# Kernel tuning notes

Measured on AMD Instinct MI355X. Metric: run time of the kernel, lower is better.

Reference implementation:

```python
import jax, jax.numpy as jnp
import numpy as np

PE_SIZE = 16

def sinusoidal_pe(d, t):
    # standard transformer sinusoidal positional encoding [t, d]
    pos = jnp.arange(t, dtype=jnp.float32)[:, None]
    div = jnp.exp(jnp.arange(0, d, 2, dtype=jnp.float32) * (-jnp.log(10000.0) / d))
    pe = jnp.zeros((t, d), dtype=jnp.float32)
    pe = pe.at[:, 0::2].set(jnp.sin(pos * div))
    pe = pe.at[:, 1::2].set(jnp.cos(pos * div))
    return pe

def setup_inputs() -> dict:
    key = jax.random.key(0)
    ks = jax.random.split(key, 12)
    B, T, N, F = 2, 256, 128, 16
    E, D, H = 1024, 128, 288
    inp = {
        'spikes': jax.random.normal(ks[0], (B, T, N, F), dtype=jnp.float32),
        'W_emb': jax.random.normal(ks[1], (F, D), dtype=jnp.float32) * (1.0 / np.sqrt(F)),
        'b_emb': jnp.zeros((D,), dtype=jnp.float32),
        'Ws1': jax.random.normal(ks[2], (D, D), dtype=jnp.float32) * (1.0 / np.sqrt(D)),
        'bs1': jnp.zeros((D,), dtype=jnp.float32),
        'Ws2': jax.random.normal(ks[3], (D, D), dtype=jnp.float32) * (1.0 / np.sqrt(D)),
        'bs2': jnp.zeros((D,), dtype=jnp.float32),
        'Wr1': jax.random.normal(ks[4], (D, D), dtype=jnp.float32) * (1.0 / np.sqrt(D)),
        'br1': jnp.zeros((D,), dtype=jnp.float32),
        'Wr2': jax.random.normal(ks[5], (D, D), dtype=jnp.float32) * (1.0 / np.sqrt(D)),
        'br2': jnp.zeros((D,), dtype=jnp.float32),
        'Wc1': jax.random.normal(ks[6], (H, H), dtype=jnp.float32) * (1.0 / np.sqrt(H)),
        'bc1': jnp.zeros((H,), dtype=jnp.float32),
        'Wc2': jax.random.normal(ks[7], (H, 5), dtype=jnp.float32) * (1.0 / np.sqrt(H)),
        'bc2': jnp.zeros((5,), dtype=jnp.float32),
        'send_edges': jax.random.randint(ks[8], (E,), 0, N, dtype=jnp.int64 if jax.config.read('jax_enable_x64') else jnp.int32),
        'recv_edges': jax.random.randint(ks[9], (E,), 0, N, dtype=jnp.int64 if jax.config.read('jax_enable_x64') else jnp.int32),
    }
    return inp

def reference(spikes, W_emb, b_emb, Ws1, bs1, Ws2, bs2, Wr1, br1, Wr2, br2,
              Wc1, bc1, Wc2, bc2, send_edges, recv_edges):
    b, t = spikes.shape[0], spikes.shape[1]
    # embedder: Linear feat->emb (shared for send/recv inputs)
    emb = spikes @ W_emb + b_emb                       # [b,t,N,D]
    # send/recv MLPs: ReLU after every Linear (2 layers)
    send = jax.nn.relu(jax.nn.relu(emb @ Ws1 + bs1) @ Ws2 + bs2)  # [b,t,N,D]
    recv = jax.nn.relu(jax.nn.relu(emb @ Wr1 + br1) @ Wr2 + br2)  # [b,t,N,D]
    # edge gather along node dim
    send_e = send[:, :, send_edges]                    # [b,t,E,D]
    recv_e = recv[:, :, recv_edges]                    # [b,t,E,D]
    # positional encoding, broadcast over batch and edges
    pe = sinusoidal_pe(PE_SIZE, t)                     # [t,PE]
    pe_b = jnp.broadcast_to(pe[None, :, None, :], (b, t, send_e.shape[2], PE_SIZE))
    send_cat = jnp.concatenate([send_e, pe_b], axis=-1)
    recv_cat = jnp.concatenate([recv_e, pe_b], axis=-1)
    # temporal offset pairing: sender at t+1, receiver at t
    full_emb = jnp.concatenate([send_cat[:, 1:], recv_cat[:, :-1]], axis=-1)  # [b,t-1,E,288]
    # combine MLP: Linear+ReLU, Linear (final bias zero-init, no activation)
    out = jax.nn.relu(full_emb @ Wc1 + bc1) @ Wc2 + bc2   # [b,t-1,E,5]
    return out
```

## Files before the change

kernel.cpp:

```cpp
#include <hip/hip_runtime.h>
#include <hip/hip_bf16.h>
#include <hip/hip_fp16.h>
#include <cstdint>
#include <cstddef>

typedef __attribute__((ext_vector_type(8))) short bf16x8;
typedef __attribute__((ext_vector_type(8))) _Float16 f16x8;
typedef __attribute__((ext_vector_type(4))) float f32x4;
typedef __attribute__((ext_vector_type(4))) unsigned u32x4;

__device__ inline unsigned short f2bf(float f) {
    __hip_bfloat16 h = __float2bfloat16(f);
    return __builtin_bit_cast(unsigned short, h);
}
__device__ inline unsigned short f2h(float f) {
    _Float16 h = (_Float16)f;
    return __builtin_bit_cast(unsigned short, h);
}
__device__ inline unsigned cvtpkrtz(float lo, float hi) {
    unsigned pk;
    asm("v_cvt_pkrtz_f16_f32 %0, %1, %2" : "=v"(pk) : "v"(lo), "v"(hi));
    return pk;
}

__global__ void prep_kernel(
    const float* __restrict__ W_emb, const float* __restrict__ b_emb,
    const float* __restrict__ Ws1, const float* __restrict__ bs1,
    const float* __restrict__ Wr1, const float* __restrict__ br1,
    const float* __restrict__ Ws2, const float* __restrict__ bs2,
    const float* __restrict__ Wr2, const float* __restrict__ br2,
    const float* __restrict__ Wc1, const float* __restrict__ bc1,
    const float* __restrict__ Wc2,
    float* __restrict__ P, float* __restrict__ bias1, float* __restrict__ bias2,
    unsigned short* __restrict__ wg1f, unsigned short* __restrict__ wg2f,
    unsigned short* __restrict__ wg3fT, unsigned short* __restrict__ wc2f)
{
    const int tid = threadIdx.x;

    if (blockIdx.x < 287) {
        __shared__ float sv[3][16], cv[3][16];
        const int base = blockIdx.x * 256;
        const int t0 = base / 288;
        if (tid < 48) {
            const int dt = tid >> 4, i = tid & 15;
            const int ii = i >> 1;
            const float div = expf(-1.1512925464970229f * (float)ii);
            const float ang = (float)(t0 + dt) * div;
            sv[dt][i] = sinf(ang);
            cv[dt][i] = cosf(ang);
        }
        __syncthreads();
        const int id = base + tid;
        if (id < 73440) {
            const int t = id / 288, ho = id % 288;
            const int dt = t - t0;
            float acc = bc1[ho];
#pragma unroll
            for (int i = 0; i < 8; i++) {
                acc += sv[dt + 1][2 * i] * Wc1[(size_t)(128 + 2 * i) * 288 + ho];
                acc += cv[dt + 1][2 * i] * Wc1[(size_t)(129 + 2 * i) * 288 + ho];
                acc += sv[dt][2 * i]     * Wc1[(size_t)(272 + 2 * i) * 288 + ho];
                acc += cv[dt][2 * i]     * Wc1[(size_t)(273 + 2 * i) * 288 + ho];
            }
            P[id] = acc;
        }
        return;
    }

    int id = (blockIdx.x - 287) * 256 + tid;

    if (id < 8192) {
        const int y = id >> 12, r = id & 4095;
        const int f = r >> 9, l = (r >> 3) & 63, j = r & 7;
        const int k = ((l >> 4) << 3) + j;
        const int n = f * 16 + (l & 15);
        float v = 0.f;
        if (k < 16) {
            const float* Wx = y ? Wr1 : Ws1;
            for (int d = 0; d < 128; d++) v += W_emb[k * 128 + d] * Wx[d * 128 + n];
        }
        wg1f[id] = f2bf(v);
        return;
    }
    id -= 8192;

    if (id < 256) {
        const int y = id >> 7, c = id & 127;
        const float* Wx = y ? Wr1 : Ws1;
        float v = (y ? br1 : bs1)[c];
        for (int d = 0; d < 128; d++) v += b_emb[d] * Wx[d * 128 + c];
        bias1[id] = v;
        return;
    }
    id -= 256;

    if (id < 32768) {
        const int y = id >> 14, r = id & 16383;
        const int f = r >> 9, l = (r >> 3) & 63, j = r & 7;
        const int ks = f >> 3, nf = f & 7;
        const int k = ks * 32 + ((l >> 4) << 3) + j;
        const int n = nf * 16 + (l & 15);
        wg2f[id] = f2bf((y ? Wr2 : Ws2)[(size_t)k * 128 + n]);
        return;
    }
    id -= 32768;

    if (id < 256) {
        bias2[id] = (id < 128) ? bs2[id] : br2[id - 128];
        return;
    }
    id -= 256;

    if (id < 73728) {
        const int p = id / 36864, r = id % 36864;
        const int frag = r >> 9, l = (r >> 3) & 63, j = r & 7;
        const int mt = frag >> 2, ks = frag & 3;
        const int k = ks * 32 + ((l >> 4) << 3) + j;
        const int n = mt * 16 + (l & 15);
        wg3fT[id] = f2bf(Wc1[(size_t)(p * 144 + k) * 288 + n]);
        return;
    }
    id -= 73728;

    if (id < 4608) {
        const int j = id & 7, l = (id >> 3) & 63, ks = id >> 9;
        const int k = ks * 32 + ((l >> 4) << 3) + j;
        const int c = l & 15;
        wc2f[id] = (c < 5) ? f2h(Wc2[(size_t)k * 5 + c]) : (unsigned short)0;
    }
}

#define H1ROWB 272
#define H1YB   34816
#define H2BASE 69632
#define SROWB  592
#define SMATB  75776
#define LDS_B2 151552

__global__ __launch_bounds__(1024) void final5(
    const float* __restrict__ spikes,
    const unsigned short* __restrict__ wg1f, const float* __restrict__ bias1,
    const unsigned short* __restrict__ wg2f, const float* __restrict__ bias2,
    const unsigned short* __restrict__ wg3fT, const float* __restrict__ Pt,
    const unsigned short* __restrict__ wc2f, const float* __restrict__ bc2,
    const int* __restrict__ se, const int* __restrict__ re,
    float* __restrict__ out)
{
    extern __shared__ unsigned char lds[];
    const int slice = blockIdx.x;
    const int b = slice / 255, t = slice % 255;
    const int tid = threadIdx.x, w = tid >> 6, l = tid & 63;
    const int lm = l & 15, lk = l >> 4;

    {
        const int y = w >> 3, rowblk = w & 7;
        const int tt = y ? t : t + 1;
        bf16x8 a0 = {0, 0, 0, 0, 0, 0, 0, 0};
        if (lk < 2) {
            const float* p = spikes +
                ((size_t)((b * 256 + tt) * 128 + rowblk * 16 + lm)) * 16 + lk * 8;
            const float4 v0 = *reinterpret_cast<const float4*>(p);
            const float4 v1 = *reinterpret_cast<const float4*>(p + 4);
            a0[0] = (short)f2bf(v0.x); a0[1] = (short)f2bf(v0.y);
            a0[2] = (short)f2bf(v0.z); a0[3] = (short)f2bf(v0.w);
            a0[4] = (short)f2bf(v1.x); a0[5] = (short)f2bf(v1.y);
            a0[6] = (short)f2bf(v1.z); a0[7] = (short)f2bf(v1.w);
        }
        f32x4 acc[8];
#pragma unroll
        for (int nf = 0; nf < 8; nf++) acc[nf] = (f32x4){0.f, 0.f, 0.f, 0.f};
#pragma unroll
        for (int nf = 0; nf < 8; nf++) {
            const bf16x8 bfr = *reinterpret_cast<const bf16x8*>(
                wg1f + y * 4096 + nf * 512 + l * 8);
            acc[nf] = __builtin_amdgcn_mfma_f32_16x16x32_bf16(a0, bfr, acc[nf], 0, 0, 0);
        }
        unsigned char* hb = lds + y * H1YB + (rowblk * 16 + lk * 4) * H1ROWB;
#pragma unroll
        for (int nf = 0; nf < 8; nf++) {
            const int c = nf * 16 + lm;
            const float add = bias1[y * 128 + c];
#pragma unroll
            for (int reg = 0; reg < 4; reg++)
                *reinterpret_cast<unsigned short*>(hb + reg * H1ROWB + c * 2) =
                    f2bf(fmaxf(acc[nf][reg] + add, 0.f));
        }
    }
    __syncthreads();

    {
        const int y = w >> 3, rowblk = w & 7;
        bf16x8 a[4];
#pragma unroll
        for (int ks = 0; ks < 4; ks++)
            a[ks] = *reinterpret_cast<const bf16x8*>(
                lds + y * H1YB + (rowblk * 16 + lm) * H1ROWB + ks * 64 + lk * 16);
        f32x4 acc[8];
#pragma unroll
        for (int nf = 0; nf < 8; nf++) acc[nf] = (f32x4){0.f, 0.f, 0.f, 0.f};
#pragma unroll
        for (int ks = 0; ks < 4; ks++)
#pragma unroll
            for (int nf = 0; nf < 8; nf++) {
                const bf16x8 bfr = *reinterpret_cast<const bf16x8*>(
                    wg2f + (size_t)y * 16384 + (size_t)(ks * 8 + nf) * 512 + l * 8);
                acc[nf] = __builtin_amdgcn_mfma_f32_16x16x32_bf16(a[ks], bfr, acc[nf], 0, 0, 0);
            }
        unsigned char* hb = lds + H2BASE + y * H1YB + (rowblk * 16 + lk * 4) * H1ROWB;
#pragma unroll
        for (int nf = 0; nf < 8; nf++) {
            const int c = nf * 16 + lm;
            const float add = bias2[y * 128 + c];
#pragma unroll
            for (int reg = 0; reg < 4; reg++)
                *reinterpret_cast<unsigned short*>(hb + reg * H1ROWB + c * 2) =
                    f2bf(fmaxf(acc[nf][reg] + add, 0.f));
        }
    }
    __syncthreads();

    const int rowg = w & 3, colg = w >> 2;
    const int p  = colg >> 1;
    const int mtb = (colg & 1) * 9;
    bf16x8 bfr[2][4];
#pragma unroll
    for (int half = 0; half < 2; half++)
#pragma unroll
        for (int ks = 0; ks < 4; ks++)
            bfr[half][ks] = *reinterpret_cast<const bf16x8*>(
                lds + H2BASE + p * H1YB +
                (rowg * 32 + half * 16 + lm) * H1ROWB + ks * 64 + lk * 16);
    f16x8 bfrag[9];
#pragma unroll
    for (int ks = 0; ks < 9; ks++)
        bfrag[ks] = *reinterpret_cast<const f16x8*>(wc2f + (ks * 64 + l) * 8);
    const float bias = (lm < 5) ? bc2[lm] : 0.f;
    __syncthreads();

    {
        unsigned char* mb0 = lds + p * SMATB + (rowg * 32 + lm) * SROWB;
        unsigned char* mb1 = mb0 + 16 * SROWB;
#pragma unroll
        for (int m9 = 0; m9 < 9; m9++) {
            const int mt = mtb + m9;
            f32x4 acc0 = {0.f, 0.f, 0.f, 0.f};
            f32x4 acc1 = {0.f, 0.f, 0.f, 0.f};
#pragma unroll
            for (int ks = 0; ks < 4; ks++) {
                const bf16x8 afr = *reinterpret_cast<const bf16x8*>(
                    wg3fT + ((size_t)(((p * 18 + mt) << 2) + ks) << 9) + l * 8);
                acc0 = __builtin_amdgcn_mfma_f32_16x16x32_bf16(afr, bfr[0][ks], acc0, 0, 0, 0);
                acc1 = __builtin_amdgcn_mfma_f32_16x16x32_bf16(afr, bfr[1][ks], acc1, 0, 0, 0);
            }
            const int c0 = mt * 16 + lk * 4;
            float4 pa = {0.f, 0.f, 0.f, 0.f};
            if (p) pa = *reinterpret_cast<const float4*>(Pt + (size_t)t * 288 + c0);
            const int boff = mt * 32 + lk * 8;
            uint2 wv;
            wv.x = cvtpkrtz(acc0[0] + pa.x, acc0[1] + pa.y);
            wv.y = cvtpkrtz(acc0[2] + pa.z, acc0[3] + pa.w);
            *reinterpret_cast<uint2*>(mb0 + boff) = wv;
            wv.x = cvtpkrtz(acc1[0] + pa.x, acc1[1] + pa.y);
            wv.y = cvtpkrtz(acc1[2] + pa.z, acc1[3] + pa.w);
            *reinterpret_cast<uint2*>(mb1 + boff) = wv;
        }
    }
    __syncthreads();

    {
        const unsigned char* sb[4];
        const unsigned char* rb[4];
#pragma unroll
        for (int it = 0; it < 4; it++) {
            const int e0 = (w * 4 + it) * 16;
            sb[it] = lds + se[e0 + lm] * SROWB + lk * 16;
            rb[it] = lds + SMATB + re[e0 + lm] * SROWB + lk * 16;
        }
        f32x4 acc[4];
#pragma unroll
        for (int it = 0; it < 4; it++) acc[it] = (f32x4){0.f, 0.f, 0.f, 0.f};

#pragma unroll
        for (int ks = 0; ks < 9; ks++) {
            u32x4 s4[4], r4[4];
#pragma unroll
            for (int it = 0; it < 4; it++) {
                s4[it] = *reinterpret_cast<const u32x4*>(sb[it] + ks * 64);
                r4[it] = *reinterpret_cast<const u32x4*>(rb[it] + ks * 64);
            }
#pragma unroll
            for (int it = 0; it < 4; it++) {
                u32x4 hw;
#pragma unroll
                for (int i = 0; i < 4; i++) {
                    unsigned hsum, hrel;
                    asm("v_pk_add_f16 %0, %1, %2" : "=v"(hsum) : "v"(s4[it][i]), "v"(r4[it][i]));
                    asm("v_pk_max_f16 %0, %1, 0"  : "=v"(hrel) : "v"(hsum));
                    hw[i] = hrel;
                }
                acc[it] = __builtin_amdgcn_mfma_f32_16x16x32_f16(
                    __builtin_bit_cast(f16x8, hw), bfrag[ks], acc[it], 0, 0, 0);
            }
        }
        if (lm < 5) {
#pragma unroll
            for (int it = 0; it < 4; it++) {
                const int e0 = (w * 4 + it) * 16;
                float* op = out + ((size_t)slice * 1024 + e0 + lk * 4) * 5 + lm;
                op[0]  = acc[it][0] + bias;
                op[5]  = acc[it][1] + bias;
                op[10] = acc[it][2] + bias;
                op[15] = acc[it][3] + bias;
            }
        }
    }
}

extern "C" void kernel_launch(void* const* d_in, const int* in_sizes, int n_in,
                              void* d_out, int out_size, void* d_ws, size_t ws_size,
                              hipStream_t stream)
{
    const float* spikes = (const float*)d_in[0];
    const float* W_emb  = (const float*)d_in[1];
    const float* b_emb  = (const float*)d_in[2];
    const float* Ws1    = (const float*)d_in[3];
    const float* bs1    = (const float*)d_in[4];
    const float* Ws2    = (const float*)d_in[5];
    const float* bs2    = (const float*)d_in[6];
    const float* Wr1    = (const float*)d_in[7];
    const float* br1    = (const float*)d_in[8];
    const float* Wr2    = (const float*)d_in[9];
    const float* br2    = (const float*)d_in[10];
    const float* Wc1    = (const float*)d_in[11];
    const float* bc1    = (const float*)d_in[12];
    const float* Wc2    = (const float*)d_in[13];
    const float* bc2    = (const float*)d_in[14];
    const int*   se     = (const int*)d_in[15];
    const int*   re     = (const int*)d_in[16];

    float* out = (float*)d_out;
    float* ws  = (float*)d_ws;

    float*          P     = ws;
    float*          bias1 = ws + 73440;
    float*          bias2 = ws + 73696;
    unsigned short* wg1f  = (unsigned short*)(ws + 73952);
    unsigned short* wg2f  = (unsigned short*)(ws + 78048);
    unsigned short* wg3fT = (unsigned short*)(ws + 94432);
    unsigned short* wc2f  = (unsigned short*)(ws + 131296);

    const dim3 blk(256);

    (void)hipFuncSetAttribute(reinterpret_cast<const void*>(final5),
                              hipFuncAttributeMaxDynamicSharedMemorySize, LDS_B2);

    prep_kernel<<<755, blk, 0, stream>>>(
        W_emb, b_emb, Ws1, bs1, Wr1, br1, Ws2, bs2, Wr2, br2, Wc1, bc1, Wc2,
        P, bias1, bias2, wg1f, wg2f, wg3fT, wc2f);

    final5<<<510, dim3(1024), LDS_B2, stream>>>(
        spikes, wg1f, bias1, wg2f, bias2, wg3fT, P, wc2f, bc2, se, re, out);
}
```

Measured before the change: 51.48 us.

## Reorder edges by LDS bank key to cut bank conflicts in gather

Adds a prep stage that ranks the edges by a key built from the low three bits of the sender and receiver node indices, then interleaves them so each 16-edge MFMA group spreads its LDS row reads across banks. The final kernel reads the permuted sender and receiver indices and scatters outputs back through the stored edge permutation. This targets LDS bank conflicts in the gather of edge rows. In exchange it adds an O(E^2) rank pass per prep block and turns the output stores into scattered, less coalesced writes.

Result: slower. 82.23 us (+59.7%).

```diff
diff --git a/kernel.cpp b/kernel.cpp
--- a/kernel.cpp
+++ b/kernel.cpp
@@ -31,9 +31,11 @@
     const float* __restrict__ Wr2, const float* __restrict__ br2,
     const float* __restrict__ Wc1, const float* __restrict__ bc1,
     const float* __restrict__ Wc2,
+    const int* __restrict__ se, const int* __restrict__ re,
     float* __restrict__ P, float* __restrict__ bias1, float* __restrict__ bias2,
     unsigned short* __restrict__ wg1f, unsigned short* __restrict__ wg2f,
-    unsigned short* __restrict__ wg3fT, unsigned short* __restrict__ wc2f)
+    unsigned short* __restrict__ wg3fT, unsigned short* __restrict__ wc2f,
+    int* __restrict__ eidx, int* __restrict__ sidx, int* __restrict__ ridx)
 {
     const int tid = threadIdx.x;
 
@@ -67,6 +69,24 @@
         return;
     }
 
+    if (blockIdx.x >= 755) {
+        __shared__ int sse[1024], sre[1024];
+        for (int i = tid; i < 1024; i += 256) { sse[i] = se[i]; sre[i] = re[i]; }
+        __syncthreads();
+        const int e = (blockIdx.x - 755) * 256 + tid;
+        const int key = ((sse[e] & 7) << 3) | (sre[e] & 7);
+        int rank = 0;
+        for (int i = 0; i < 1024; i++) {
+            const int ki = ((sse[i] & 7) << 3) | (sre[i] & 7);
+            rank += (ki < key) || (ki == key && i < e);
+        }
+        const int slot = ((rank & 63) << 4) | (rank >> 6);
+        eidx[slot] = e;
+        sidx[slot] = sse[e];
+        ridx[slot] = sre[e];
+        return;
+    }
+
     int id = (blockIdx.x - 287) * 256 + tid;
 
     if (id < 8192) {
@@ -143,8 +163,8 @@
     const unsigned short* __restrict__ wg2f, const float* __restrict__ bias2,
     const unsigned short* __restrict__ wg3fT, const float* __restrict__ Pt,
     const unsigned short* __restrict__ wc2f, const float* __restrict__ bc2,
-    const int* __restrict__ se, const int* __restrict__ re,
-    float* __restrict__ out)
+    const int* __restrict__ eidx, const int* __restrict__ sidx,
+    const int* __restrict__ ridx, float* __restrict__ out)
 {
     extern __shared__ unsigned char lds[];
     const int slice = blockIdx.x;
@@ -235,6 +255,13 @@
     for (int ks = 0; ks < 9; ks++)
         bfrag[ks] = *reinterpret_cast<const f16x8*>(wc2f + (ks * 64 + l) * 8);
     const float bias = (lm < 5) ? bc2[lm] : 0.f;
+    int srw[4], rrw[4];
+#pragma unroll
+    for (int it = 0; it < 4; it++) {
+        const int base = (w * 4 + it) * 16 + lm;
+        srw[it] = sidx[base];
+        rrw[it] = ridx[base];
+    }
     __syncthreads();
 
     {
@@ -268,14 +295,6 @@
     __syncthreads();
 
     {
-        const unsigned char* sb[4];
-        const unsigned char* rb[4];
-#pragma unroll
-        for (int it = 0; it < 4; it++) {
-            const int e0 = (w * 4 + it) * 16;
-            sb[it] = lds + se[e0 + lm] * SROWB + lk * 16;
-            rb[it] = lds + SMATB + re[e0 + lm] * SROWB + lk * 16;
-        }
         f32x4 acc[4];
 #pragma unroll
         for (int it = 0; it < 4; it++) acc[it] = (f32x4){0.f, 0.f, 0.f, 0.f};
@@ -285,8 +304,10 @@
             u32x4 s4[4], r4[4];
 #pragma unroll
             for (int it = 0; it < 4; it++) {
-                s4[it] = *reinterpret_cast<const u32x4*>(sb[it] + ks * 64);
-                r4[it] = *reinterpret_cast<const u32x4*>(rb[it] + ks * 64);
+                s4[it] = *reinterpret_cast<const u32x4*>(
+                    lds + srw[it] * SROWB + lk * 16 + ks * 64);
+                r4[it] = *reinterpret_cast<const u32x4*>(
+                    lds + SMATB + rrw[it] * SROWB + lk * 16 + ks * 64);
             }
 #pragma unroll
             for (int it = 0; it < 4; it++) {
@@ -305,12 +326,12 @@
         if (lm < 5) {
 #pragma unroll
             for (int it = 0; it < 4; it++) {
-                const int e0 = (w * 4 + it) * 16;
-                float* op = out + ((size_t)slice * 1024 + e0 + lk * 4) * 5 + lm;
-                op[0]  = acc[it][0] + bias;
-                op[5]  = acc[it][1] + bias;
-                op[10] = acc[it][2] + bias;
-                op[15] = acc[it][3] + bias;
+                const int base = (w * 4 + it) * 16 + lk * 4;
+#pragma unroll
+                for (int reg = 0; reg < 4; reg++) {
+                    const int edge = eidx[base + reg];
+                    out[((size_t)slice * 1024 + edge) * 5 + lm] = acc[it][reg] + bias;
+                }
             }
         }
     }
@@ -348,16 +369,20 @@
     unsigned short* wg2f  = (unsigned short*)(ws + 78048);
     unsigned short* wg3fT = (unsigned short*)(ws + 94432);
     unsigned short* wc2f  = (unsigned short*)(ws + 131296);
+    int*            eidx  = (int*)(ws + 133600);
+    int*            sidx  = (int*)(ws + 134624);
+    int*            ridx  = (int*)(ws + 135648);
 
     const dim3 blk(256);
 
     (void)hipFuncSetAttribute(reinterpret_cast<const void*>(final5),
                               hipFuncAttributeMaxDynamicSharedMemorySize, LDS_B2);
 
-    prep_kernel<<<755, blk, 0, stream>>>(
+    prep_kernel<<<759, blk, 0, stream>>>(
         W_emb, b_emb, Ws1, bs1, Wr1, br1, Ws2, bs2, Wr2, br2, Wc1, bc1, Wc2,
-        P, bias1, bias2, wg1f, wg2f, wg3fT, wc2f);
+        se, re, P, bias1, bias2, wg1f, wg2f, wg3fT, wc2f, eidx, sidx, ridx);
 
     final5<<<510, dim3(1024), LDS_B2, stream>>>(
-        spikes, wg1f, bias1, wg2f, bias2, wg3fT, P, wc2f, bc2, se, re, out);
-}
+        spikes, wg1f, bias1, wg2f, bias2, wg3fT, P, wc2f, bc2,
+        eidx, sidx, ridx, out);
+}
```
